# Performance work log

Hardware: AMD Instinct MI355X
Metric: run time of the kernel (lower is better)

## Reference

```python
import jax, jax.numpy as jnp
import numpy as np
import jax.scipy.linalg as jsl

K = 4           # num_hops + 1
N = 4096        # nodes
D = 256         # in_dim == out_dim
S = 32          # subspace_dim
ETA = 0.5
EPS = 0.5


def setup_inputs() -> dict:
    key = jax.random.key(0)
    k1, k2, k3 = jax.random.split(key, 3)
    hops = jax.random.normal(k1, (K, N, D), dtype=jnp.float32)
    A = (jax.random.uniform(k2, (N, N)) < 0.01).astype(jnp.float32)
    A = jnp.maximum(A, A.T)
    A = jnp.fill_diagonal(A, 1.0, inplace=False)
    deg = A.sum(axis=1)
    L = jnp.diag(deg) - A  # graph Laplacian
    # orthonormal subspace bases via QR, as in __init__
    raw = jax.random.normal(k3, (K, D, S), dtype=jnp.float32)
    q, _ = jnp.linalg.qr(raw)
    U = q[:, :, :S]
    hop_weights = jnp.ones((K,), dtype=jnp.float32) / K
    threshold = jnp.full((D,), 0.05, dtype=jnp.float32)
    lambda_lap = jnp.asarray(0.1, dtype=jnp.float32)
    return {"hops": hops, "adj_mask": A, "L": L, "U": U,
            "hop_weights": hop_weights, "threshold": threshold,
            "lambda_lap": lambda_lap}


def reference(hops, adj_mask, L, U, hop_weights, threshold, lambda_lap):
    n = hops.shape[1]
    s = U.shape[-1]
    w = jax.nn.softmax(hop_weights, axis=0)
    mask_add = (1.0 - adj_mask) * -1e9  # [n, n]
    I_s = jnp.eye(s, dtype=hops.dtype)
    agg_total = jnp.zeros((hops.shape[2], n), dtype=hops.dtype)  # [d, n]
    coeff = s / (n * EPS ** 2)
    for k in range(K):  # small fixed hop count
        Uk = U[k]                      # [d, s]
        Zk = Uk.T @ hops[k].T          # [s, n]
        M_k = I_s + coeff * (Zk @ Zk.T)  # [s, s]
        cf = jsl.cho_factor(M_k)
        M_inv = jsl.cho_solve(cf, I_s)   # Cholesky inverse
        MZ = M_inv @ Zk                  # [s, n]
        scores = Zk.T @ MZ + mask_add    # [n, n] Mahalanobis-style attention
        alpha = jax.nn.softmax(scores, axis=1)
        grad_k = Uk @ (MZ @ alpha.T)     # [d, n]
        agg_total = agg_total + w[k] * grad_k
    H_agg = agg_total.T                  # [n, d]
    lap_grad = lambda_lap * (L @ H_agg)
    H_half = hops[0] + ETA * H_agg - ETA * lap_grad
    # soft-threshold (proximal step); in_dim == out_dim so no proj
    H_out = jnp.sign(H_half) * jax.nn.relu(jnp.abs(H_half) - threshold[None, :])
    # orthogonality regularizer over subspace bases
    orth_loss = jnp.asarray(0.0, dtype=hops.dtype)
    for k in range(K):
        UkTUk = U[k].T @ U[k]
        orth_loss = orth_loss + ((UkTUk - I_s) ** 2).sum()
        for l in range(k + 1, K):
            orth_loss = orth_loss + ((U[k].T @ U[l]) ** 2).sum()
    lap_smooth = jnp.sum(H_out * (L @ H_out))  # trace(H^T L H)
    return (H_out, orth_loss, lap_smooth, jax.lax.stop_gradient(w))
```

## Files before the change

kernel.cpp:

```cpp
#include <hip/hip_runtime.h>
#include <cstddef>

typedef unsigned short ushortt;
typedef unsigned int uintt;

static constexpr int Nn = 4096;
static constexpr int Dd = 256;
static constexpr int Ss = 32;
static constexpr int Kk = 4;
static constexpr int CAP = 144;
static constexpr int RST = 136;
static constexpr float kEta   = 0.5f;
static constexpr float kCoeff = 0.03125f;

__device__ __forceinline__ float waveReduceSum(float v){
  #pragma unroll
  for (int off = 32; off > 0; off >>= 1) v += __shfl_down(v, off, 64);
  return v;
}
__device__ __forceinline__ float blo(uintt u){ return __uint_as_float(u << 16); }
__device__ __forceinline__ float bhi(uintt u){ return __uint_as_float(u & 0xffff0000u); }
__device__ __forceinline__ ushortt f2b(float x){
  uintt u = __float_as_uint(x);
  uintt r = (u + 0x7fffu + ((u >> 16) & 1u)) >> 16;
  return (ushortt)r;
}
__device__ __forceinline__ float b2f(ushortt u){ return __uint_as_float(((uintt)u) << 16); }

__global__ __launch_bounds__(256) void buildz_kernel(const float* __restrict__ A,
                                                     const float* __restrict__ hw,
                                                     const float* __restrict__ hops,
                                                     const float* __restrict__ U,
                                                     int* __restrict__ deg,
                                                     int* __restrict__ colx,
                                                     float* __restrict__ Zt4,
                                                     float* __restrict__ Ubt,
                                                     float* __restrict__ out){
  int tid = threadIdx.x;
  if (blockIdx.x >= Nn){
    int b = blockIdx.x - Nn;
    int k = b >> 9;
    int i0 = (b & 511) * 8;
    __shared__ float Us[Ss][132];
    int s = tid & 31, ii = tid >> 5;
    int i = i0 + ii;
    float acc = 0.f;
    #pragma unroll
    for (int chunk = 0; chunk < 2; chunk++){
      for (int t = tid; t < 128 * 32; t += 256){
        int dl = t >> 5, s2 = t & 31;
        Us[s2][dl] = U[(size_t)k * Dd * Ss + (size_t)(chunk * 128 + dl) * Ss + s2];
      }
      __syncthreads();
      const float4* u4 = (const float4*)(&Us[s][0]);
      const float4* h4 = (const float4*)(hops + ((size_t)k * Nn + i) * Dd) + chunk * 32;
      #pragma unroll 8
      for (int dq = 0; dq < 32; dq++){
        float4 h = h4[dq];
        float4 u = u4[dq];
        acc += h.x*u.x + h.y*u.y + h.z*u.z + h.w*u.w;
      }
      __syncthreads();
    }
    Zt4[(size_t)i * 128 + k * 32 + s] = acc;
    if (b < 128){
      int idx = b * 256 + tid;
      int c = idx >> 8, d = idx & 255;
      int kk = c >> 5, s2 = c & 31;
      Ubt[idx] = U[(size_t)kk * Dd * Ss + (size_t)d * Ss + s2];
    }
    return;
  }
  int i = blockIdx.x;
  if (i == 0 && tid == 0){
    out[1048576] = 0.f;
    out[1048577] = 0.f;
    float a0=hw[0], a1=hw[1], a2=hw[2], a3=hw[3];
    float mx = fmaxf(fmaxf(a0,a1), fmaxf(a2,a3));
    float e0=expf(a0-mx), e1=expf(a1-mx), e2=expf(a2-mx), e3=expf(a3-mx);
    float s = e0+e1+e2+e3;
    out[1048578]=e0/s; out[1048579]=e1/s; out[1048580]=e2/s; out[1048581]=e3/s;
  }
  int lane = tid & 63, w = tid >> 6;
  __shared__ int wbuf[4][96];
  __shared__ int wcnt[4];
  const float4* row4 = (const float4*)(A + (size_t)i * Nn);
  int cnt = 0;
  int base = w * 256;
  unsigned long long below = (lane == 63) ? 0x7fffffffffffffffull : ((1ull << lane) - 1ull);
  #pragma unroll
  for (int it = 0; it < 4; it++){
    int c4 = base + it * 64 + lane;
    float4 v = row4[c4];
    bool f0 = (v.x != 0.f), f1 = (v.y != 0.f), f2 = (v.z != 0.f), f3 = (v.w != 0.f);
    unsigned long long m0 = __ballot(f0), m1 = __ballot(f1),
                       m2 = __ballot(f2), m3 = __ballot(f3);
    int pre = __popcll(m0 & below) + __popcll(m1 & below)
            + __popcll(m2 & below) + __popcll(m3 & below);
    int pos = cnt + pre;
    int j0 = c4 * 4;
    if (f0){ if (pos < 96) wbuf[w][pos] = j0;     pos++; }
    if (f1){ if (pos < 96) wbuf[w][pos] = j0 + 1; pos++; }
    if (f2){ if (pos < 96) wbuf[w][pos] = j0 + 2; pos++; }
    if (f3){ if (pos < 96) wbuf[w][pos] = j0 + 3; pos++; }
    cnt += __popcll(m0) + __popcll(m1) + __popcll(m2) + __popcll(m3);
  }
  if (cnt > 96) cnt = 96;
  if (lane == 0) wcnt[w] = cnt;
  __syncthreads();
  int off = 0;
  for (int ww = 0; ww < w; ww++) off += wcnt[ww];
  int total = wcnt[0] + wcnt[1] + wcnt[2] + wcnt[3];
  for (int idx = lane; idx < cnt; idx += 64){
    int p = off + idx;
    if (p < CAP) colx[(size_t)i * CAP + p] = wbuf[w][idx];
  }
  if (tid == 0) deg[i] = (total < CAP) ? total : CAP;
}

__global__ __launch_bounds__(256) void mpart_kernel(const float* __restrict__ Zt4,
                                                    float* __restrict__ Mpart){
  int b = blockIdx.x;
  int k = b >> 4, ch = b & 15;
  int i0 = ch * 256;
  __shared__ float zs[256][33];
  for (int t = threadIdx.x; t < 256 * 32; t += 256){
    int ii = t >> 5, s = t & 31;
    zs[ii][s] = Zt4[(size_t)(i0 + ii) * 128 + k * 32 + s];
  }
  __syncthreads();
  int tid = threadIdx.x;
  int s2 = tid & 31, s1b = tid >> 5;
  float a0=0.f, a1=0.f, a2=0.f, a3=0.f;
  for (int ii = 0; ii < 256; ii++){
    float zc = zs[ii][s2];
    a0 = fmaf(zs[ii][s1b],      zc, a0);
    a1 = fmaf(zs[ii][8 + s1b],  zc, a1);
    a2 = fmaf(zs[ii][16 + s1b], zc, a2);
    a3 = fmaf(zs[ii][24 + s1b], zc, a3);
  }
  float* outp = Mpart + (size_t)b * 1024;
  outp[0 * 256 + tid] = a0;
  outp[1 * 256 + tid] = a1;
  outp[2 * 256 + tid] = a2;
  outp[3 * 256 + tid] = a3;
}

__global__ __launch_bounds__(256) void inv_kernel(const float* __restrict__ Mpart,
                                                  float* __restrict__ Minv){
  __shared__ float Msh[4][32][33];
  int tid = threadIdx.x;
  for (int e = tid; e < 4096; e += 256){
    int k = e >> 10, rc = e & 1023;
    float s = 0.f;
    for (int ch = 0; ch < 16; ch++) s += Mpart[(size_t)(k * 16 + ch) * 1024 + rc];
    int r = rc >> 5, c = rc & 31;
    Msh[k][r][c] = kCoeff * s + ((r == c) ? 1.f : 0.f);
  }
  __syncthreads();
  int k = tid >> 6, lane = tid & 63, r = lane & 31, half = lane >> 5;
  float a[32];
  #pragma unroll
  for (int j = 0; j < 32; j++) a[j] = half ? ((r == j) ? 1.f : 0.f) : Msh[k][r][j];
  #pragma unroll
  for (int p = 0; p < 32; p++){
    float app = __shfl(a[p], p, 64);
    float pinv = 1.f / app;
    float f = __shfl(a[p], r, 64);
    #pragma unroll
    for (int j = 0; j < 32; j++){
      float pr = __shfl(a[j], p + (half << 5), 64) * pinv;
      a[j] = (r == p) ? pr : fmaf(-f, pr, a[j]);
    }
  }
  if (half){
    #pragma unroll
    for (int j = 0; j < 32; j++) Minv[(size_t)k * 1024 + r * 32 + j] = a[j];
  }
}

__global__ __launch_bounds__(256) void mz_kernel(const float* __restrict__ Zt4,
                                                 const float* __restrict__ Minv,
                                                 ushortt* __restrict__ MZb){
  int b = blockIdx.x;
  int k = b >> 7;
  int i0 = (b & 127) * 32;
  __shared__ float mi[32][33];
  __shared__ float zs[32][33];
  for (int t = threadIdx.x; t < 1024; t += 256){
    int ii = t >> 5, s2 = t & 31;
    mi[ii][s2] = Minv[(size_t)k * 1024 + t];
    zs[ii][s2] = Zt4[(size_t)(i0 + ii) * 128 + k * 32 + s2];
  }
  __syncthreads();
  int s = threadIdx.x & 31;
  for (int rr = 0; rr < 4; rr++){
    int ii = rr * 8 + (threadIdx.x >> 5);
    float acc = 0.f;
    #pragma unroll
    for (int s2 = 0; s2 < 32; s2++) acc = fmaf(mi[s][s2], zs[ii][s2], acc);
    MZb[(size_t)(i0 + ii) * 128 + k * 32 + s] = f2b(acc);
  }
}

__global__ __launch_bounds__(256) void agg_kernel(const float* __restrict__ Zt4,
                                                  const ushortt* __restrict__ MZb,
                                                  const float* __restrict__ wvec,
                                                  const int* __restrict__ deg,
                                                  const int* __restrict__ colx,
                                                  float* __restrict__ Vw){
  int i = blockIdx.x, tid = threadIdx.x;
  int lane = tid & 63, k = tid >> 6;
  __shared__ __align__(16) ushortt rows[CAP * RST];
  __shared__ int cols[CAP];
  __shared__ __align__(16) float zi[128];
  __shared__ float sc[4][CAP + 8];
  int m = deg[i];
  if (tid < 128) zi[tid] = Zt4[(size_t)i * 128 + tid];
  if (tid < m)  cols[tid] = colx[(size_t)i * CAP + tid];
  __syncthreads();

  int q = tid & 3, r = tid >> 2;
  float zq[32];
  {
    const float4* z4 = (const float4*)(&zi[q * 32]);
    #pragma unroll
    for (int p = 0; p < 8; p++){
      float4 z = z4[p];
      zq[p*4+0]=z.x; zq[p*4+1]=z.y; zq[p*4+2]=z.z; zq[p*4+3]=z.w;
    }
  }

  for (int t = r; t < m; t += 64){
    int j = cols[t];
    const uint4* src = (const uint4*)(MZb + (size_t)j * 128 + q * 32);
    uint4 q0 = src[0], q1 = src[1], q2 = src[2], q3 = src[3];
    uint4* dst = (uint4*)(rows + (size_t)t * RST + q * 32);
    dst[0] = q0; dst[1] = q1; dst[2] = q2; dst[3] = q3;
    float acc = 0.f;
    acc += blo(q0.x)*zq[0] + bhi(q0.x)*zq[1] + blo(q0.y)*zq[2] + bhi(q0.y)*zq[3];
    acc += blo(q0.z)*zq[4] + bhi(q0.z)*zq[5] + blo(q0.w)*zq[6] + bhi(q0.w)*zq[7];
    acc += blo(q1.x)*zq[8] + bhi(q1.x)*zq[9] + blo(q1.y)*zq[10]+ bhi(q1.y)*zq[11];
    acc += blo(q1.z)*zq[12]+ bhi(q1.z)*zq[13]+ blo(q1.w)*zq[14]+ bhi(q1.w)*zq[15];
    acc += blo(q2.x)*zq[16]+ bhi(q2.x)*zq[17]+ blo(q2.y)*zq[18]+ bhi(q2.y)*zq[19];
    acc += blo(q2.z)*zq[20]+ bhi(q2.z)*zq[21]+ blo(q2.w)*zq[22]+ bhi(q2.w)*zq[23];
    acc += blo(q3.x)*zq[24]+ bhi(q3.x)*zq[25]+ blo(q3.y)*zq[26]+ bhi(q3.y)*zq[27];
    acc += blo(q3.z)*zq[28]+ bhi(q3.z)*zq[29]+ blo(q3.w)*zq[30]+ bhi(q3.w)*zq[31];
    sc[q][t] = acc;
  }
  __syncthreads();

  float lmax = -3.0e38f;
  for (int t = lane; t < m; t += 64) lmax = fmaxf(lmax, sc[k][t]);
  #pragma unroll
  for (int off = 32; off > 0; off >>= 1) lmax = fmaxf(lmax, __shfl_xor(lmax, off, 64));
  float lsum = 0.f;
  for (int t = lane; t < m; t += 64){
    float e = __expf(sc[k][t] - lmax);
    sc[k][t] = e;
    lsum += e;
  }
  #pragma unroll
  for (int off = 32; off > 0; off >>= 1) lsum += __shfl_xor(lsum, off, 64);
  float scale = wvec[k] / lsum;

  int c2 = lane & 15, h = lane >> 4;
  float a0 = 0.f, a1 = 0.f;
  #pragma unroll 4
  for (int t = h; t < m; t += 4){
    uintt u = *(const uintt*)(rows + (size_t)t * RST + k * 32 + c2 * 2);
    float e = sc[k][t];
    a0 = fmaf(blo(u), e, a0);
    a1 = fmaf(bhi(u), e, a1);
  }
  a0 += __shfl_xor(a0, 16, 64); a0 += __shfl_xor(a0, 32, 64);
  a1 += __shfl_xor(a1, 16, 64); a1 += __shfl_xor(a1, 32, 64);
  if (h == 0){
    float2 v2 = make_float2(a0 * scale, a1 * scale);
    *(float2*)(Vw + (size_t)i * 128 + k * 32 + c2 * 2) = v2;
  }
}

__global__ __launch_bounds__(256) void gho_kernel(const float* __restrict__ Vw,
                                                  const float* __restrict__ Ubt,
                                                  const float* __restrict__ hops0,
                                                  const float* __restrict__ thr,
                                                  const float* __restrict__ U,
                                                  const float* __restrict__ lam_ptr,
                                                  const int* __restrict__ deg,
                                                  const int* __restrict__ colx,
                                                  float* __restrict__ out,
                                                  ushortt* __restrict__ Hb){
  int tid = threadIdx.x;
  if (blockIdx.x >= 1024){
    int g = (blockIdx.x - 1024) * 256 + tid;
    int pair = g >> 10;
    int idx = g & 1023;
    int s1 = idx >> 5, s2 = idx & 31;
    const int pk_[10] = {0,0,0,0,1,1,1,2,2,3};
    const int pl_[10] = {0,1,2,3,1,2,3,2,3,3};
    int pk = pk_[pair], pl = pl_[pair];
    const float* Uk = U + (size_t)pk * Dd * Ss;
    const float* Ul = U + (size_t)pl * Dd * Ss;
    float dot = 0.f;
    for (int d = 0; d < Dd; d++) dot += Uk[d * Ss + s1] * Ul[d * Ss + s2];
    float val = dot - ((pk == pl && s1 == s2) ? 1.f : 0.f);
    val *= val;
    val = waveReduceSum(val);
    __shared__ float redo[4];
    if ((tid & 63) == 0) redo[tid >> 6] = val;
    __syncthreads();
    if (tid == 0) atomicAdd(out + 1048576, redo[0] + redo[1] + redo[2] + redo[3]);
    return;
  }
  int i0 = blockIdx.x * 4;
  int lane = tid & 63, w = tid >> 6;
  __shared__ float Cs[4][132];
  __shared__ int cols_s[4][CAP];
  {
    int i = i0 + w;
    int m = deg[i];
    for (int t = lane; t < m; t += 64) cols_s[w][t] = colx[(size_t)i * CAP + t];
    float lam = lam_ptr[0];
    int half = lane >> 5, c32 = lane & 31;
    float4 acc = make_float4(0.f, 0.f, 0.f, 0.f);
    for (int t = half; t < m; t += 2){
      int j = cols_s[w][t];
      float4 v = ((const float4*)(Vw + (size_t)j * 128))[c32];
      acc.x += v.x; acc.y += v.y; acc.z += v.z; acc.w += v.w;
    }
    acc.x += __shfl_xor(acc.x, 32, 64);
    acc.y += __shfl_xor(acc.y, 32, 64);
    acc.z += __shfl_xor(acc.z, 32, 64);
    acc.w += __shfl_xor(acc.w, 32, 64);
    if (half == 0){
      float4 self = ((const float4*)(Vw + (size_t)i * 128))[c32];
      float ca = kEta * (1.f - lam * (float)m);
      float cb = kEta * lam;
      float4 o;
      o.x = fmaf(ca, self.x, cb * acc.x);
      o.y = fmaf(ca, self.y, cb * acc.y);
      o.z = fmaf(ca, self.z, cb * acc.z);
      o.w = fmaf(ca, self.w, cb * acc.w);
      *(float4*)(&Cs[w][c32 * 4]) = o;
    }
  }
  __syncthreads();
  int d4 = tid & 63, g = tid >> 6;
  float4 acc = make_float4(0.f, 0.f, 0.f, 0.f);
  #pragma unroll 4
  for (int c = 0; c < 128; c++){
    float4 ub = ((const float4*)(Ubt + (size_t)c * 256))[d4];
    float cs = Cs[g][c];
    acc.x = fmaf(cs, ub.x, acc.x);
    acc.y = fmaf(cs, ub.y, acc.y);
    acc.z = fmaf(cs, ub.z, acc.z);
    acc.w = fmaf(cs, ub.w, acc.w);
  }
  float4 th = ((const float4*)thr)[d4];
  int i = i0 + g;
  float4 hp = ((const float4*)(hops0 + (size_t)i * 256))[d4];
  float hx = hp.x + acc.x, hy = hp.y + acc.y;
  float hz = hp.z + acc.z, hw = hp.w + acc.w;
  float4 o;
  o.x = copysignf(fmaxf(fabsf(hx) - th.x, 0.f), hx);
  o.y = copysignf(fmaxf(fabsf(hy) - th.y, 0.f), hy);
  o.z = copysignf(fmaxf(fabsf(hz) - th.z, 0.f), hz);
  o.w = copysignf(fmaxf(fabsf(hw) - th.w, 0.f), hw);
  ((float4*)(out + (size_t)i * 256))[d4] = o;
  ushort4 hb;
  hb.x = f2b(o.x); hb.y = f2b(o.y); hb.z = f2b(o.z); hb.w = f2b(o.w);
  *((ushort4*)(Hb + (size_t)i * 256 + d4 * 4)) = hb;
}

__global__ __launch_bounds__(256) void lap_kernel(const float* __restrict__ Hout,
                                                  const ushortt* __restrict__ Hb,
                                                  const int* __restrict__ deg,
                                                  const int* __restrict__ colx,
                                                  float* __restrict__ lap_part){
  int b = blockIdx.x;
  int i = b >> 1, half = b & 1;
  int tid = threadIdx.x;
  int dl = tid & 127, g = tid >> 7;
  int d = half * 128 + dl;
  __shared__ int cols[CAP];
  int m = deg[i];
  if (tid < m) cols[tid] = colx[(size_t)i * CAP + tid];
  __syncthreads();
  float nb = 0.f;
  #pragma unroll 8
  for (int t = g; t < m; t += 2)
    nb += b2f(Hb[(size_t)cols[t] * 256 + d]);
  float hi = Hout[(size_t)i * 256 + d];
  float part = -hi * nb;
  if (g == 0) part = fmaf((float)m * hi, hi, part);
  part = waveReduceSum(part);
  __shared__ float red[4];
  if ((tid & 63) == 0) red[tid >> 6] = part;
  __syncthreads();
  if (tid == 0) lap_part[b] = red[0] + red[1] + red[2] + red[3];
}

__global__ __launch_bounds__(256) void lapred_kernel(const float* __restrict__ lap_part,
                                                     float* __restrict__ out){
  int tid = threadIdx.x;
  float s = 0.f;
  const float4* p4 = (const float4*)lap_part;
  #pragma unroll
  for (int q = 0; q < 8; q++){
    float4 v = p4[q * 256 + tid];
    s += v.x + v.y + v.z + v.w;
  }
  s = waveReduceSum(s);
  __shared__ float red[4];
  if ((tid & 63) == 0) red[tid >> 6] = s;
  __syncthreads();
  if (tid == 0) out[1048577] = red[0] + red[1] + red[2] + red[3];
}

extern "C" void kernel_launch(void* const* d_in, const int* in_sizes, int n_in,
                              void* d_out, int out_size, void* d_ws, size_t ws_size,
                              hipStream_t stream)
{
  const float* hops = (const float*)d_in[0];
  const float* A    = (const float*)d_in[1];
  const float* L    = (const float*)d_in[2];
  const float* U    = (const float*)d_in[3];
  const float* hw   = (const float*)d_in[4];
  const float* thr  = (const float*)d_in[5];
  const float* lam  = (const float*)d_in[6];
  (void)L; (void)in_sizes; (void)n_in; (void)out_size; (void)ws_size;

  float* out = (float*)d_out;
  float* ws  = (float*)d_ws;

  float*   Zt4   = ws;
  float*   Vw    = ws + 524288;
  ushortt* MZb   = (ushortt*)(ws + 1572864);
  ushortt* Hb    = (ushortt*)(ws + 1835008);
  float*   Ubt   = ws + 2359296;
  float*   Mpart = ws + 2392064;
  float*   Minv  = ws + 2457600;
  int*     deg   = (int*)(ws + 2461696);
  int*     colx  = (int*)(ws + 2465792);
  float*   lapp  = ws + 3121152;

  float* w_out = out + 1048578;

  buildz_kernel<<<Nn + Kk*512, 256, 0, stream>>>(A, hw, hops, U, deg, colx, Zt4, Ubt, out);
  mpart_kernel <<<Kk*16, 256, 0, stream>>>(Zt4, Mpart);
  inv_kernel   <<<1, 256, 0, stream>>>(Mpart, Minv);
  mz_kernel    <<<Kk*128, 256, 0, stream>>>(Zt4, Minv, MZb);
  agg_kernel   <<<Nn, 256, 0, stream>>>(Zt4, MZb, w_out, deg, colx, Vw);
  gho_kernel   <<<1064, 256, 0, stream>>>(Vw, Ubt, hops, thr, U, lam, deg, colx, out, Hb);
  lap_kernel   <<<2*Nn, 256, 0, stream>>>(out, Hb, deg, colx, lapp);
  lapred_kernel<<<1, 256, 0, stream>>>(lapp, out);
}
```

Baseline: 301.2 us.

## Fold Minv into agg kernel via symmetric reassociation, drop mz_kernel

Removes the separate MZ = Minv·Z kernel. Because Minv is symmetric, scores become (Minv z_i)·z_j and the output becomes Minv·(sum alpha z_j). The agg kernel now applies Minv once per row, before the scores and after the weighted sum, and gathers bf16 Z written directly by buildz. This saves a launch and a full pass over the intermediate, at the cost of two extra small matvecs and an extra sync per row block. It also staggers the dq loop start per lane in buildz, likely to spread LDS bank accesses.

```diff
diff --git a/kernel.cpp b/kernel.cpp
--- a/kernel.cpp
+++ b/kernel.cpp
@@ -34,6 +34,7 @@
                                                      int* __restrict__ deg,
                                                      int* __restrict__ colx,
                                                      float* __restrict__ Zt4,
+                                                     ushortt* __restrict__ Zb,
                                                      float* __restrict__ Ubt,
                                                      float* __restrict__ out){
   int tid = threadIdx.x;
@@ -55,7 +56,8 @@
       const float4* u4 = (const float4*)(&Us[s][0]);
       const float4* h4 = (const float4*)(hops + ((size_t)k * Nn + i) * Dd) + chunk * 32;
       #pragma unroll 8
-      for (int dq = 0; dq < 32; dq++){
+      for (int dq0 = 0; dq0 < 32; dq0++){
+        int dq = (dq0 + s) & 31;
         float4 h = h4[dq];
         float4 u = u4[dq];
         acc += h.x*u.x + h.y*u.y + h.z*u.z + h.w*u.w;
@@ -63,6 +65,7 @@
       __syncthreads();
     }
     Zt4[(size_t)i * 128 + k * 32 + s] = acc;
+    Zb [(size_t)i * 128 + k * 32 + s] = f2b(acc);
     if (b < 128){
       int idx = b * 256 + tid;
       int c = idx >> 8, d = idx & 255;
@@ -179,32 +182,9 @@
   }
 }
 
-__global__ __launch_bounds__(256) void mz_kernel(const float* __restrict__ Zt4,
-                                                 const float* __restrict__ Minv,
-                                                 ushortt* __restrict__ MZb){
-  int b = blockIdx.x;
-  int k = b >> 7;
-  int i0 = (b & 127) * 32;
-  __shared__ float mi[32][33];
-  __shared__ float zs[32][33];
-  for (int t = threadIdx.x; t < 1024; t += 256){
-    int ii = t >> 5, s2 = t & 31;
-    mi[ii][s2] = Minv[(size_t)k * 1024 + t];
-    zs[ii][s2] = Zt4[(size_t)(i0 + ii) * 128 + k * 32 + s2];
-  }
-  __syncthreads();
-  int s = threadIdx.x & 31;
-  for (int rr = 0; rr < 4; rr++){
-    int ii = rr * 8 + (threadIdx.x >> 5);
-    float acc = 0.f;
-    #pragma unroll
-    for (int s2 = 0; s2 < 32; s2++) acc = fmaf(mi[s][s2], zs[ii][s2], acc);
-    MZb[(size_t)(i0 + ii) * 128 + k * 32 + s] = f2b(acc);
-  }
-}
-
 __global__ __launch_bounds__(256) void agg_kernel(const float* __restrict__ Zt4,
-                                                  const ushortt* __restrict__ MZb,
+                                                  const ushortt* __restrict__ Zb,
+                                                  const float* __restrict__ Minv,
                                                   const float* __restrict__ wvec,
                                                   const int* __restrict__ deg,
                                                   const int* __restrict__ colx,
@@ -214,16 +194,34 @@
   __shared__ __align__(16) ushortt rows[CAP * RST];
   __shared__ int cols[CAP];
   __shared__ __align__(16) float zi[128];
+  __shared__ __align__(16) float zim[128];
+  __shared__ __align__(16) float vsh[128];
+  __shared__ float scl[4];
   __shared__ float sc[4][CAP + 8];
   int m = deg[i];
   if (tid < 128) zi[tid] = Zt4[(size_t)i * 128 + tid];
   if (tid < m)  cols[tid] = colx[(size_t)i * CAP + tid];
   __syncthreads();
 
+  if (tid < 128){
+    int kk = tid >> 5, s = tid & 31;
+    const float4* mrow = (const float4*)(Minv + (size_t)kk * 1024 + s * 32);
+    const float4* zv   = (const float4*)(&zi[kk * 32]);
+    float a = 0.f;
+    #pragma unroll
+    for (int q2 = 0; q2 < 8; q2++){
+      float4 mr = mrow[q2];
+      float4 z  = zv[q2];
+      a += mr.x*z.x + mr.y*z.y + mr.z*z.z + mr.w*z.w;
+    }
+    zim[tid] = a;
+  }
+  __syncthreads();
+
   int q = tid & 3, r = tid >> 2;
   float zq[32];
   {
-    const float4* z4 = (const float4*)(&zi[q * 32]);
+    const float4* z4 = (const float4*)(&zim[q * 32]);
     #pragma unroll
     for (int p = 0; p < 8; p++){
       float4 z = z4[p];
@@ -233,7 +231,7 @@
 
   for (int t = r; t < m; t += 64){
     int j = cols[t];
-    const uint4* src = (const uint4*)(MZb + (size_t)j * 128 + q * 32);
+    const uint4* src = (const uint4*)(Zb + (size_t)j * 128 + q * 32);
     uint4 q0 = src[0], q1 = src[1], q2 = src[2], q3 = src[3];
     uint4* dst = (uint4*)(rows + (size_t)t * RST + q * 32);
     dst[0] = q0; dst[1] = q1; dst[2] = q2; dst[3] = q3;
@@ -262,7 +260,7 @@
   }
   #pragma unroll
   for (int off = 32; off > 0; off >>= 1) lsum += __shfl_xor(lsum, off, 64);
-  float scale = wvec[k] / lsum;
+  if (lane == 0) scl[k] = wvec[k] / lsum;
 
   int c2 = lane & 15, h = lane >> 4;
   float a0 = 0.f, a1 = 0.f;
@@ -276,8 +274,23 @@
   a0 += __shfl_xor(a0, 16, 64); a0 += __shfl_xor(a0, 32, 64);
   a1 += __shfl_xor(a1, 16, 64); a1 += __shfl_xor(a1, 32, 64);
   if (h == 0){
-    float2 v2 = make_float2(a0 * scale, a1 * scale);
-    *(float2*)(Vw + (size_t)i * 128 + k * 32 + c2 * 2) = v2;
+    vsh[k * 32 + c2 * 2]     = a0;
+    vsh[k * 32 + c2 * 2 + 1] = a1;
+  }
+  __syncthreads();
+
+  if (tid < 128){
+    int kk = tid >> 5, s = tid & 31;
+    const float4* mrow = (const float4*)(Minv + (size_t)kk * 1024 + s * 32);
+    const float4* vv   = (const float4*)(&vsh[kk * 32]);
+    float a = 0.f;
+    #pragma unroll
+    for (int q2 = 0; q2 < 8; q2++){
+      float4 mr = mrow[q2];
+      float4 v  = vv[q2];
+      a += mr.x*v.x + mr.y*v.y + mr.z*v.z + mr.w*v.w;
+    }
+    Vw[(size_t)i * 128 + tid] = scl[kk] * a;
   }
 }
 
@@ -436,7 +449,7 @@
 
   float*   Zt4   = ws;
   float*   Vw    = ws + 524288;
-  ushortt* MZb   = (ushortt*)(ws + 1572864);
+  ushortt* Zb    = (ushortt*)(ws + 1572864);
   ushortt* Hb    = (ushortt*)(ws + 1835008);
   float*   Ubt   = ws + 2359296;
   float*   Mpart = ws + 2392064;
@@ -447,11 +460,10 @@
 
   float* w_out = out + 1048578;
 
-  buildz_kernel<<<Nn + Kk*512, 256, 0, stream>>>(A, hw, hops, U, deg, colx, Zt4, Ubt, out);
+  buildz_kernel<<<Nn + Kk*512, 256, 0, stream>>>(A, hw, hops, U, deg, colx, Zt4, Zb, Ubt, out);
   mpart_kernel <<<Kk*16, 256, 0, stream>>>(Zt4, Mpart);
   inv_kernel   <<<1, 256, 0, stream>>>(Mpart, Minv);
-  mz_kernel    <<<Kk*128, 256, 0, stream>>>(Zt4, Minv, MZb);
-  agg_kernel   <<<Nn, 256, 0, stream>>>(Zt4, MZb, w_out, deg, colx, Vw);
+  agg_kernel   <<<Nn, 256, 0, stream>>>(Zt4, Zb, Minv, w_out, deg, colx, Vw);
   gho_kernel   <<<1064, 256, 0, stream>>>(Vw, Ubt, hops, thr, U, lam, deg, colx, out, Hb);
   lap_kernel   <<<2*Nn, 256, 0, stream>>>(out, Hb, deg, colx, lapp);
   lapred_kernel<<<1, 256, 0, stream>>>(lapp, out);
```

Result: no change. 305.9 us (+1.6%).
